# Optimization experiments

Measured on AMD Instinct MI355X. Metric: run time of the kernel, lower is better.

## Reference

```python
import math
import jax, jax.numpy as jnp
import numpy as np

N_HEAD = 8
BLOCK_SIZE = 1024
LN_EPS = 1e-5


def _layer_norm(x, g, b):
    mu = jnp.mean(x, axis=-1, keepdims=True)
    var = jnp.var(x, axis=-1, keepdims=True)
    return (x - mu) * jax.lax.rsqrt(var + LN_EPS) * g + b


def _skew(QEr):
    # QEr: (B, nh, L, L) -> pad one zero column on the left, reshape, drop first row
    B, nh, nr, nc = QEr.shape
    padded = jnp.pad(QEr, ((0, 0), (0, 0), (0, 0), (1, 0)))  # (B, nh, nr, nc+1)
    reshaped = padded.reshape(B, nh, nc + 1, nr)
    return reshaped[:, :, 1:, :]  # (B, nh, nr, nc)


def _attn(x, W_qkv, b_qkv, W_o, b_o, Er):
    B, L, D = x.shape
    hs = D // N_HEAD
    qkv = x @ W_qkv + b_qkv  # (B, L, 3D)
    q, k, v = jnp.split(qkv, 3, axis=-1)
    # (B, nh, L, hs)
    q = q.reshape(B, L, N_HEAD, hs).transpose(0, 2, 1, 3)
    k = k.reshape(B, L, N_HEAD, hs).transpose(0, 2, 1, 3)
    v = v.reshape(B, L, N_HEAD, hs).transpose(0, 2, 1, 3)
    start = BLOCK_SIZE - L
    Er_t = Er[start:, :].T  # (hs, L)
    QEr = q @ Er_t  # (B, nh, L, L)
    Srel = _skew(QEr)
    scores = (jnp.einsum('bhqd,bhkd->bhqk', q, k) + Srel) * (1.0 / math.sqrt(hs))
    causal = jnp.tril(jnp.ones((L, L), dtype=bool))
    scores = jnp.where(causal, scores, jnp.float32(-jnp.inf))
    att = jax.nn.softmax(scores, axis=-1)
    y = jnp.einsum('bhqk,bhkd->bhqd', att, v)
    y = y.transpose(0, 2, 1, 3).reshape(B, L, D)
    return y @ W_o + b_o


def reference(x, W_qkv, b_qkv, W_o, b_o, Er, ln1_g, ln1_b, ln2_g, ln2_b,
              W_fc, b_fc, W_proj, b_proj):
    x = x + _attn(_layer_norm(x, ln1_g, ln1_b), W_qkv, b_qkv, W_o, b_o, Er)
    h = _layer_norm(x, ln2_g, ln2_b) @ W_fc + b_fc
    h = jax.nn.gelu(h, approximate=False)
    h = h @ W_proj + b_proj
    return x + h


def setup_inputs() -> dict:
    key = jax.random.key(0)
    ks = jax.random.split(key, 8)
    B, L, D, F = 8, 1024, 1024, 4096
    hs = D // N_HEAD
    s = lambda fan_in: 1.0 / math.sqrt(fan_in)
    return {
        'x': jax.random.normal(ks[0], (B, L, D), dtype=jnp.float32),
        'W_qkv': jax.random.normal(ks[1], (D, 3 * D), dtype=jnp.float32) * s(D),
        'b_qkv': jnp.zeros((3 * D,), dtype=jnp.float32),
        'W_o': jax.random.normal(ks[2], (D, D), dtype=jnp.float32) * s(D),
        'b_o': jnp.zeros((D,), dtype=jnp.float32),
        'Er': jax.random.normal(ks[3], (BLOCK_SIZE, hs), dtype=jnp.float32),
        'ln1_g': jnp.ones((D,), dtype=jnp.float32),
        'ln1_b': jnp.zeros((D,), dtype=jnp.float32),
        'ln2_g': jnp.ones((D,), dtype=jnp.float32),
        'ln2_b': jnp.zeros((D,), dtype=jnp.float32),
        'W_fc': jax.random.normal(ks[4], (D, F), dtype=jnp.float32) * s(D),
        'b_fc': jnp.zeros((F,), dtype=jnp.float32),
        'W_proj': jax.random.normal(ks[5], (F, D), dtype=jnp.float32) * s(F),
        'b_proj': jnp.zeros((D,), dtype=jnp.float32),
    }
```

## Files before the change

kernel.cpp:

```cpp
#include <hip/hip_runtime.h>
#include <hip/hip_bf16.h>
#include <math.h>

#define BB 8
#define LL 1024
#define DD 1024
#define FF 4096
#define NHH 8
#define HSS 128
#define SCALE 0.08838834764831845f
#define TRI(qi, kt) ((qi) * ((qi) + 1) / 2 + (kt))

typedef __bf16 bf16;
typedef __bf16 bf16x8 __attribute__((ext_vector_type(8)));
typedef float f32x4 __attribute__((ext_vector_type(4)));
typedef _Float16 f16;
typedef _Float16 f16x4 __attribute__((ext_vector_type(4)));

__device__ inline void async_copy16(const void* g, void* l) {
  __builtin_amdgcn_global_load_lds(
      (const __attribute__((address_space(1))) unsigned int*)g,
      (__attribute__((address_space(3))) unsigned int*)l, 16, 0, 0);
}

__global__ __launch_bounds__(256)
void transpose_cast_kernel(const float* __restrict__ W, bf16* __restrict__ Wt,
                           int K, int N) {
  __shared__ float tile[32][33];
  int n0 = blockIdx.x * 32, k0 = blockIdx.y * 32;
  int tx = threadIdx.x, ty = threadIdx.y;
#pragma unroll
  for (int i = 0; i < 32; i += 8)
    tile[ty + i][tx] = W[(size_t)(k0 + ty + i) * N + n0 + tx];
  __syncthreads();
#pragma unroll
  for (int i = 0; i < 32; i += 8)
    Wt[(size_t)(n0 + ty + i) * K + k0 + tx] = (bf16)tile[tx][ty + i];
}

__global__ __launch_bounds__(256)
void pack_er_kernel(const float* __restrict__ Er, bf16* __restrict__ ErP) {
  int g = blockIdx.x, tid = threadIdx.x;
  int l15 = tid & 15, quad = (tid >> 4) & 3, st = tid >> 6;
  const float* src = Er + (size_t)(g * 16 + l15) * HSS + st * 32 + quad * 8;
  bf16* dst = ErP + (size_t)g * 2048 + tid * 8;
#pragma unroll
  for (int j = 0; j < 8; j++) dst[j] = (bf16)src[j];
}

__global__ __launch_bounds__(256)
void ln_kernel(const float* __restrict__ x, const float* __restrict__ g,
               const float* __restrict__ bta, bf16* __restrict__ out) {
  int row = blockIdx.x;
  int tid = threadIdx.x;
  const float4 v = ((const float4*)(x + (size_t)row * DD))[tid];
  float s = v.x + v.y + v.z + v.w;
  float s2 = v.x * v.x + v.y * v.y + v.z * v.z + v.w * v.w;
#pragma unroll
  for (int o = 32; o > 0; o >>= 1) {
    s += __shfl_down(s, o);
    s2 += __shfl_down(s2, o);
  }
  __shared__ float a1[4], a2[4];
  int wave = tid >> 6;
  if ((tid & 63) == 0) { a1[wave] = s; a2[wave] = s2; }
  __syncthreads();
  s = a1[0] + a1[1] + a1[2] + a1[3];
  s2 = a2[0] + a2[1] + a2[2] + a2[3];
  float mu = s * (1.0f / DD);
  float rstd = rsqrtf(s2 * (1.0f / DD) - mu * mu + 1e-5f);
  float4 gv = ((const float4*)g)[tid];
  float4 bv = ((const float4*)bta)[tid];
  bf16* o4 = out + (size_t)row * DD + tid * 4;
  o4[0] = (bf16)((v.x - mu) * rstd * gv.x + bv.x);
  o4[1] = (bf16)((v.y - mu) * rstd * gv.y + bv.y);
  o4[2] = (bf16)((v.z - mu) * rstd * gv.z + bv.z);
  o4[3] = (bf16)((v.w - mu) * rstd * gv.w + bv.w);
}

template <int EPI>
__global__ __launch_bounds__(256)
void gemm_kernel(const bf16* __restrict__ A, const bf16* __restrict__ Bt,
                 const float* __restrict__ bias, const float* __restrict__ res,
                 void* __restrict__ Cout, int M, int N, int K) {
  __shared__ bf16 Als[128 * 64];
  __shared__ bf16 Bls[128 * 64];
  int tid = threadIdx.x;
  int wave = tid >> 6, lane = tid & 63;
  int l15 = lane & 15, quad = lane >> 4;

  int m0 = blockIdx.y * 128, n0 = blockIdx.x * 128;
  int wm = (wave >> 1) * 64, wn = (wave & 1) * 64;
  f32x4 acc[4][4] = {};

  const bf16* asrc[4];
  const bf16* bsrc[4];
  int ldso[4];
#pragma unroll
  for (int i = 0; i < 4; i++) {
    int u = i * 256 + tid;
    int row = u >> 3, c = u & 7;
    int g = c ^ (row & 7);
    asrc[i] = A + (size_t)(m0 + row) * K + g * 8;
    bsrc[i] = Bt + (size_t)(n0 + row) * K + g * 8;
    ldso[i] = u * 8;
  }

  for (int k0 = 0; k0 < K; k0 += 64) {
    __syncthreads();
#pragma unroll
    for (int i = 0; i < 4; i++) {
      async_copy16(asrc[i] + k0, &Als[ldso[i]]);
      async_copy16(bsrc[i] + k0, &Bls[ldso[i]]);
    }
    __syncthreads();

    bf16x8 af[2][4], bfr[2][4];
#pragma unroll
    for (int kk = 0; kk < 2; kk++) {
#pragma unroll
      for (int mt = 0; mt < 4; mt++) {
        int ra = wm + mt * 16 + l15;
        af[kk][mt] = *(const bf16x8*)&Als[ra * 64 + (((kk * 4 + quad) ^ (ra & 7)) << 3)];
        int rb = wn + mt * 16 + l15;
        bfr[kk][mt] = *(const bf16x8*)&Bls[rb * 64 + (((kk * 4 + quad) ^ (rb & 7)) << 3)];
      }
    }
#pragma unroll
    for (int kk = 0; kk < 2; kk++)
#pragma unroll
      for (int mt = 0; mt < 4; mt++)
#pragma unroll
        for (int nt = 0; nt < 4; nt++)
          acc[mt][nt] = __builtin_amdgcn_mfma_f32_16x16x32_bf16(af[kk][mt], bfr[kk][nt],
                                                                acc[mt][nt], 0, 0, 0);
  }

#pragma unroll
  for (int mt = 0; mt < 4; mt++) {
#pragma unroll
    for (int nt = 0; nt < 4; nt++) {
      int col = n0 + wn + nt * 16 + l15;
      float bv = bias[col];
#pragma unroll
      for (int r = 0; r < 4; r++) {
        int row = m0 + wm + mt * 16 + quad * 4 + r;
        float v = acc[mt][nt][r] + bv;
        if (EPI == 1) v = 0.5f * v * (1.0f + erff(v * 0.7071067811865475f));
        if (EPI == 2) {
          v += res[(size_t)row * N + col];
          ((float*)Cout)[(size_t)row * N + col] = v;
        } else {
          ((bf16*)Cout)[(size_t)row * N + col] = (bf16)v;
        }
      }
    }
  }
}

__global__ __launch_bounds__(256)
void pack_kv_kernel(const bf16* __restrict__ qkv, bf16* __restrict__ Kpack,
                    bf16* __restrict__ Vpack) {
  __shared__ bf16 Vst[64][132];
  int kt = blockIdx.x, h = blockIdx.y, b = blockIdx.z;
  int tid = threadIdx.x;
  const size_t rs = 3 * DD;
  const bf16* kb = qkv + (size_t)b * LL * rs + (size_t)(kt * 64) * rs + DD + h * HSS;
  const bf16* vb = kb + DD;
  bf16* kp = Kpack + ((size_t)(b * NHH + h) * 16 + kt) * (64 * 128);
  bf16* vp = Vpack + ((size_t)(b * NHH + h) * 16 + kt) * (128 * 64);
#pragma unroll
  for (int i = 0; i < 4; i++) {
    int u = i * 256 + tid;
    int kk = u >> 4, c = u & 15;
    bf16x8 kv = *(const bf16x8*)(kb + (size_t)kk * rs + c * 8);
    *(bf16x8*)(kp + kk * 128 + ((c ^ kk) & 15) * 8) = kv;
    *(bf16x8*)&Vst[kk][c * 8] = *(const bf16x8*)(vb + (size_t)kk * rs + c * 8);
  }
  __syncthreads();
#pragma unroll
  for (int i = 0; i < 4; i++) {
    int u = i * 256 + tid;
    int d = u >> 3, c = u & 7;
    bf16x8 t;
#pragma unroll
    for (int j = 0; j < 8; j++) t[j] = Vst[c * 8 + j][d];
    *(bf16x8*)(vp + d * 64 + ((c ^ (d & 7))) * 8) = t;
  }
}

__global__ __launch_bounds__(256)
void relband_kernel(const bf16* __restrict__ qkv, const bf16* __restrict__ ErP,
                    f16* __restrict__ band) {
  int tid = threadIdx.x, wave = tid >> 6, lane = tid & 63;
  int l15 = lane & 15, quad = lane >> 4;
  int h = blockIdx.y, b = blockIdx.z;
  const size_t rs = 3 * DD;
  const bf16* qbase = qkv + (size_t)b * LL * rs + h * HSS;
  f16* bbase = band + (size_t)(b * NHH + h) * (136 * 4096);

#pragma unroll 1
  for (int ph = 0; ph < 2; ph++) {
    int qb = ph ? 15 - blockIdx.x : blockIdx.x;
    int qw0 = qb * 64 + wave * 16;

    bf16x8 qf[4];
#pragma unroll
    for (int st = 0; st < 4; st++)
      qf[st] = *(const bf16x8*)(qbase + (size_t)(qw0 + l15) * rs + st * 32 + quad * 8);

#pragma unroll 1
    for (int kt = 0; kt <= qb; kt++) {
      int k0 = kt * 64;
      int kmax_off = qw0 + 15 - k0;
      int m_base = 1008 - qw0 + k0;
      int gb = m_base >> 4;
      int ntR = (kmax_off >> 4) + 1;
      if (ntR > 4) ntR = 4;

      f32x4 rr[5] = {};
#pragma unroll
      for (int n = 0; n < 5; n++) {
        if (n <= ntR) {
          int g = gb + n;
          if (g > 63) g = 63;
          const bf16* ep = ErP + (size_t)g * 2048 + lane * 8;
#pragma unroll
          for (int st = 0; st < 4; st++) {
            bf16x8 ef = *(const bf16x8*)(ep + st * 512);
            rr[n] = __builtin_amdgcn_mfma_f32_16x16x32_bf16(qf[st], ef, rr[n], 0, 0, 0);
          }
        }
      }

      f16x4 sf[4];
#pragma unroll
      for (int rg = 0; rg < 4; rg++) {
        int qloc = quad * 4 + rg;
        int tt = 15 - qloc + l15;
        int src = (lane & 48) | (tt & 15);
        float shv[5];
#pragma unroll
        for (int n = 0; n < 5; n++)
          shv[n] = (n <= ntR) ? __shfl(rr[n][rg], src) : 0.f;
#pragma unroll
        for (int nt = 0; nt < 4; nt++)
          sf[nt][rg] = (f16)((tt & 16) ? shv[nt + 1] : shv[nt]);
      }
      f16* tb = bbase + (size_t)TRI(qb, kt) * 4096;
#pragma unroll
      for (int nt = 0; nt < 4; nt++)
        if (nt * 16 <= kmax_off)
          *(f16x4*)(tb + (wave * 4 + nt) * 256 + l15 * 16 + quad * 4) = sf[nt];
    }
  }
}

__global__ __launch_bounds__(256)
void flash_kernel(const bf16* __restrict__ qkv, const bf16* __restrict__ Kpack,
                  const bf16* __restrict__ Vpack, const f16* __restrict__ band,
                  bf16* __restrict__ y) {
  __shared__ bf16 Kls[2][64 * 128];
  __shared__ bf16 Vls[2][128 * 64];
  __shared__ bf16 Pls[4][16][72];

  int tid = threadIdx.x, wave = tid >> 6, lane = tid & 63;
  int l15 = lane & 15, quad = lane >> 4;
  int h = blockIdx.y, b = blockIdx.z;

  const size_t rs = 3 * DD;
  const bf16* qbase = qkv + (size_t)b * LL * rs + h * HSS;
  const bf16* kp = Kpack + (size_t)(b * NHH + h) * 16 * (64 * 128);
  const bf16* vp = Vpack + (size_t)(b * NHH + h) * 16 * (128 * 64);
  const f16* bnd = band + (size_t)(b * NHH + h) * (136 * 4096);

  int buf = 0;
#pragma unroll 1
  for (int ph = 0; ph < 2; ph++) {
    int qb = ph ? 15 - blockIdx.x : blockIdx.x;
    int qw0 = qb * 64 + wave * 16;
    int nkt = qb + 1;

    bf16x8 qf[4];
#pragma unroll
    for (int st = 0; st < 4; st++)
      qf[st] = *(const bf16x8*)(qbase + (size_t)(qw0 + l15) * rs + st * 32 + quad * 8);

    {
      const bf16* ks = kp;
      const bf16* vs = vp;
#pragma unroll
      for (int i = 0; i < 4; i++) {
        int off = (wave * 4 + i) * 512 + lane * 8;
        async_copy16(ks + off, &Kls[buf][off]);
        async_copy16(vs + off, &Vls[buf][off]);
      }
    }

    f32x4 o[8] = {};
    float mrow[4] = {-INFINITY, -INFINITY, -INFINITY, -INFINITY};
    float lrow[4] = {0.f, 0.f, 0.f, 0.f};

#pragma unroll 1
    for (int kt = 0; kt < nkt; kt++) {
      int k0 = kt * 64;
      int kmax_off = qw0 + 15 - k0;
      __syncthreads();

      const f16* tb = bnd + (size_t)TRI(qb, kt) * 4096;
      f16x4 srl[4] = {};
#pragma unroll
      for (int nt = 0; nt < 4; nt++)
        if (nt * 16 <= kmax_off)
          srl[nt] = *(const f16x4*)(tb + (wave * 4 + nt) * 256 + l15 * 16 + quad * 4);

      if (kt + 1 < nkt) {
        const bf16* ks = kp + (size_t)(kt + 1) * (64 * 128);
        const bf16* vs = vp + (size_t)(kt + 1) * (128 * 64);
#pragma unroll
        for (int i = 0; i < 4; i++) {
          int off = (wave * 4 + i) * 512 + lane * 8;
          async_copy16(ks + off, &Kls[buf ^ 1][off]);
          async_copy16(vs + off, &Vls[buf ^ 1][off]);
        }
      }

      f32x4 sa[4] = {};
#pragma unroll
      for (int nt = 0; nt < 4; nt++) {
        if (nt * 16 <= kmax_off) {
          int kk = nt * 16 + l15;
#pragma unroll
          for (int st = 0; st < 4; st++) {
            bf16x8 kf = *(const bf16x8*)&Kls[buf][kk * 128 + (((st * 4 + quad) ^ l15) & 15) * 8];
            sa[nt] = __builtin_amdgcn_mfma_f32_16x16x32_bf16(qf[st], kf, sa[nt], 0, 0, 0);
          }
        }
      }

      float pmx[4] = {-INFINITY, -INFINITY, -INFINITY, -INFINITY};
#pragma unroll
      for (int nt = 0; nt < 4; nt++) {
        if (nt * 16 <= kmax_off) {
          int kg = k0 + nt * 16 + l15;
#pragma unroll
          for (int rg = 0; rg < 4; rg++) {
            int qg = qw0 + quad * 4 + rg;
            float v = (sa[nt][rg] + (float)srl[nt][rg]) * SCALE;
            v = (kg <= qg) ? v : -INFINITY;
            sa[nt][rg] = v;
            pmx[rg] = fmaxf(pmx[rg], v);
          }
        } else {
#pragma unroll
          for (int rg = 0; rg < 4; rg++) sa[nt][rg] = -INFINITY;
        }
      }

#pragma unroll
      for (int rg = 0; rg < 4; rg++) {
        float v = pmx[rg];
        v = fmaxf(v, __shfl_xor(v, 1));
        v = fmaxf(v, __shfl_xor(v, 2));
        v = fmaxf(v, __shfl_xor(v, 4));
        v = fmaxf(v, __shfl_xor(v, 8));
        float mnew = fmaxf(mrow[rg], v);
        float alpha = __expf(mrow[rg] - mnew);
        mrow[rg] = mnew;
        lrow[rg] *= alpha;
#pragma unroll
        for (int nt = 0; nt < 8; nt++) o[nt][rg] *= alpha;
        pmx[rg] = mnew;
      }
      float ls[4] = {0.f, 0.f, 0.f, 0.f};
#pragma unroll
      for (int nt = 0; nt < 4; nt++)
#pragma unroll
        for (int rg = 0; rg < 4; rg++) {
          float p = __expf(sa[nt][rg] - pmx[rg]);
          ls[rg] += p;
          Pls[wave][quad * 4 + rg][nt * 16 + l15] = (bf16)p;
        }
#pragma unroll
      for (int rg = 0; rg < 4; rg++) {
        float v = ls[rg];
        v += __shfl_xor(v, 1);
        v += __shfl_xor(v, 2);
        v += __shfl_xor(v, 4);
        v += __shfl_xor(v, 8);
        lrow[rg] += v;
      }

      bf16x8 pf[2];
#pragma unroll
      for (int s2 = 0; s2 < 2; s2++)
        pf[s2] = *(const bf16x8*)&Pls[wave][l15][s2 * 32 + quad * 8];
#pragma unroll
      for (int nt = 0; nt < 8; nt++) {
        int d = nt * 16 + l15;
#pragma unroll
        for (int s2 = 0; s2 < 2; s2++) {
          if (s2 * 32 <= kmax_off) {
            bf16x8 vf = *(const bf16x8*)&Vls[buf][d * 64 + (((s2 * 4 + quad) ^ (l15 & 7)) & 7) * 8];
            o[nt] = __builtin_amdgcn_mfma_f32_16x16x32_bf16(pf[s2], vf, o[nt], 0, 0, 0);
          }
        }
      }
      buf ^= 1;
    }

#pragma unroll
    for (int rg = 0; rg < 4; rg++) {
      float inv = 1.0f / lrow[rg];
      int qg = qw0 + quad * 4 + rg;
      bf16* yr = y + ((size_t)b * LL + qg) * DD + h * HSS;
#pragma unroll
      for (int nt = 0; nt < 8; nt++) yr[nt * 16 + l15] = (bf16)(o[nt][rg] * inv);
    }
  }
}

extern "C" void kernel_launch(void* const* d_in, const int* in_sizes, int n_in,
                              void* d_out, int out_size, void* d_ws, size_t ws_size,
                              hipStream_t stream) {
  const float* x = (const float*)d_in[0];
  const float* W_qkv = (const float*)d_in[1];
  const float* b_qkv = (const float*)d_in[2];
  const float* W_o = (const float*)d_in[3];
  const float* b_o = (const float*)d_in[4];
  const float* Er = (const float*)d_in[5];
  const float* ln1_g = (const float*)d_in[6];
  const float* ln1_b = (const float*)d_in[7];
  const float* ln2_g = (const float*)d_in[8];
  const float* ln2_b = (const float*)d_in[9];
  const float* W_fc = (const float*)d_in[10];
  const float* b_fc = (const float*)d_in[11];
  const float* W_proj = (const float*)d_in[12];
  const float* b_proj = (const float*)d_in[13];
  float* out = (float*)d_out;

  char* p = (char*)d_ws;
  auto alloc = [&](size_t bytes) {
    char* r = p;
    p += (bytes + 255) & ~(size_t)255;
    return r;
  };
  bf16* Wt_qkv = (bf16*)alloc((size_t)3072 * 1024 * 2);
  bf16* Wt_o   = (bf16*)alloc((size_t)1024 * 1024 * 2);
  bf16* Wt_fc  = (bf16*)alloc((size_t)4096 * 1024 * 2);
  bf16* Wt_pr  = (bf16*)alloc((size_t)1024 * 4096 * 2);
  bf16* ErP    = (bf16*)alloc((size_t)1024 * 128 * 2);
  bf16* xn     = (bf16*)alloc((size_t)8192 * 1024 * 2);
  bf16* qkvb   = (bf16*)alloc((size_t)8192 * 3072 * 2);
  bf16* yb     = (bf16*)alloc((size_t)8192 * 1024 * 2);
  bf16* Kpack  = (bf16*)alloc((size_t)64 * 16 * 64 * 128 * 2);
  bf16* Vpack  = (bf16*)alloc((size_t)64 * 16 * 128 * 64 * 2);
  f16*  band   = (f16*)alloc((size_t)64 * 136 * 4096 * 2);
  float* x2    = (float*)band;
  bf16* hb     = qkvb;

  transpose_cast_kernel<<<dim3(3072 / 32, 1024 / 32), dim3(32, 8), 0, stream>>>(W_qkv, Wt_qkv, 1024, 3072);
  transpose_cast_kernel<<<dim3(1024 / 32, 1024 / 32), dim3(32, 8), 0, stream>>>(W_o, Wt_o, 1024, 1024);
  transpose_cast_kernel<<<dim3(4096 / 32, 1024 / 32), dim3(32, 8), 0, stream>>>(W_fc, Wt_fc, 1024, 4096);
  transpose_cast_kernel<<<dim3(1024 / 32, 4096 / 32), dim3(32, 8), 0, stream>>>(W_proj, Wt_pr, 4096, 1024);
  pack_er_kernel<<<64, 256, 0, stream>>>(Er, ErP);

  ln_kernel<<<8192, 256, 0, stream>>>(x, ln1_g, ln1_b, xn);
  gemm_kernel<0><<<dim3(24, 64), 256, 0, stream>>>(xn, Wt_qkv, b_qkv, nullptr, qkvb, 8192, 3072, 1024);
  pack_kv_kernel<<<dim3(16, 8, 8), 256, 0, stream>>>(qkvb, Kpack, Vpack);
  relband_kernel<<<dim3(8, 8, 8), 256, 0, stream>>>(qkvb, ErP, band);
  flash_kernel<<<dim3(8, 8, 8), 256, 0, stream>>>(qkvb, Kpack, Vpack, band, yb);
  gemm_kernel<2><<<dim3(8, 64), 256, 0, stream>>>(yb, Wt_o, b_o, x, x2, 8192, 1024, 1024);
  ln_kernel<<<8192, 256, 0, stream>>>(x2, ln2_g, ln2_b, xn);
  gemm_kernel<1><<<dim3(32, 64), 256, 0, stream>>>(xn, Wt_fc, b_fc, nullptr, hb, 8192, 4096, 1024);
  gemm_kernel<2><<<dim3(8, 64), 256, 0, stream>>>(hb, Wt_pr, b_proj, x2, out, 8192, 1024, 4096);
}
```

Measured before the change: 616.5 us.

## Add 256x256-tile 8-wave GEMM with ping-pong LDS staging for QKV and FC

Introduces a new GEMM kernel using 256x256 output tiles, 512 threads and double-buffered LDS. It interleaves async global-to-LDS loads of quarter tiles with MFMA phases, using explicit vmcnt waits, barriers and setprio. The kernel replaces the 128x128 GEMM for the QKV projection and the FC+GELU projection, aiming for more data reuse per tile and better overlap of loads with compute. The cost is a large LDS footprint (128KB) and register pressure, which may limit occupancy. Grid sizes also drop, to 384 and 512 blocks.

```diff
diff --git a/kernel.cpp b/kernel.cpp
--- a/kernel.cpp
+++ b/kernel.cpp
@@ -22,6 +22,10 @@
       (const __attribute__((address_space(1))) unsigned int*)g,
       (__attribute__((address_space(3))) unsigned int*)l, 16, 0, 0);
 }
+
+#define FENCE() asm volatile("" ::: "memory")
+#define BARRIER() do { FENCE(); __builtin_amdgcn_s_barrier(); FENCE(); } while (0)
+#define VMCNT6() asm volatile("s_waitcnt vmcnt(6)" ::: "memory")
 
 __global__ __launch_bounds__(256)
 void transpose_cast_kernel(const float* __restrict__ W, bf16* __restrict__ Wt,
@@ -76,6 +80,122 @@
   o4[1] = (bf16)((v.y - mu) * rstd * gv.y + bv.y);
   o4[2] = (bf16)((v.z - mu) * rstd * gv.z + bv.z);
   o4[3] = (bf16)((v.w - mu) * rstd * gv.w + bv.w);
+}
+
+template <int EPI>
+__global__ __launch_bounds__(512)
+void gemm256_kernel(const bf16* __restrict__ A, const bf16* __restrict__ Bt,
+                    const float* __restrict__ bias, void* __restrict__ Cout,
+                    int M, int N, int K) {
+  __shared__ bf16 Als[2][256 * 64];
+  __shared__ bf16 Bls[2][256 * 64];
+  int tid = threadIdx.x;
+  int wave = tid >> 6, lane = tid & 63;
+  int l15 = lane & 15, quad = lane >> 4;
+  int wmi = wave >> 2, wni = wave & 3;
+  int m0 = blockIdx.y * 256, n0 = blockIdx.x * 256;
+
+  int u0 = tid, u1 = tid + 512;
+  int r0 = u0 >> 3, c0 = ((u0 & 7) ^ (r0 & 7)) << 3;
+  int r1 = u1 >> 3, c1 = ((u1 & 7) ^ (r1 & 7)) << 3;
+  const bf16* aB0 = A + (size_t)(m0 + r0) * K + c0;
+  const bf16* aB1 = A + (size_t)(m0 + r1) * K + c1;
+  const bf16* bB0 = Bt + (size_t)(n0 + r0) * K + c0;
+  const bf16* bB1 = Bt + (size_t)(n0 + r1) * K + c1;
+  int d0 = u0 * 8, d1 = u1 * 8;
+
+  auto stageA = [&](int b, int h, int t) {
+    size_t off = (size_t)h * 128 * K + (size_t)t * 64;
+    async_copy16(aB0 + off, &Als[b][h * 8192 + d0]);
+    async_copy16(aB1 + off, &Als[b][h * 8192 + d1]);
+  };
+  auto stageB = [&](int b, int h, int t) {
+    size_t off = (size_t)h * 128 * K + (size_t)t * 64;
+    async_copy16(bB0 + off, &Bls[b][h * 8192 + d0]);
+    async_copy16(bB1 + off, &Bls[b][h * 8192 + d1]);
+  };
+
+  f32x4 acc[8][4] = {};
+  bf16x8 af[2][4], bfr[2][2];
+
+  auto readA = [&](int b, int qm) {
+#pragma unroll
+    for (int kk = 0; kk < 2; kk++)
+#pragma unroll
+      for (int mt = 0; mt < 4; mt++) {
+        int ra = qm * 128 + wmi * 64 + mt * 16 + l15;
+        af[kk][mt] = *(const bf16x8*)&Als[b][ra * 64 + (((kk * 4 + quad) ^ (ra & 7)) << 3)];
+      }
+  };
+  auto readB = [&](int b, int qn) {
+#pragma unroll
+    for (int kk = 0; kk < 2; kk++)
+#pragma unroll
+      for (int nt = 0; nt < 2; nt++) {
+        int rb = qn * 128 + wni * 32 + nt * 16 + l15;
+        bfr[kk][nt] = *(const bf16x8*)&Bls[b][rb * 64 + (((kk * 4 + quad) ^ (rb & 7)) << 3)];
+      }
+  };
+  auto mfma16 = [&](int qm, int qn) {
+    __builtin_amdgcn_s_setprio(1);
+#pragma unroll
+    for (int kk = 0; kk < 2; kk++)
+#pragma unroll
+      for (int mt = 0; mt < 4; mt++)
+#pragma unroll
+        for (int nt = 0; nt < 2; nt++)
+          acc[qm * 4 + mt][qn * 2 + nt] = __builtin_amdgcn_mfma_f32_16x16x32_bf16(
+              af[kk][mt], bfr[kk][nt], acc[qm * 4 + mt][qn * 2 + nt], 0, 0, 0);
+    __builtin_amdgcn_s_setprio(0);
+  };
+
+  int nk = K >> 6;
+  stageA(0, 0, 0); stageB(0, 0, 0); stageB(0, 1, 0); stageA(0, 1, 0);
+  stageA(1, 0, 1); stageB(1, 1, 1);
+  VMCNT6();
+  BARRIER();
+
+  for (int t = 0; t < nk; t++) {
+    int cur = t & 1;
+    readA(cur, 0); readB(cur, 0);
+    if (t + 1 < nk) stageB(cur ^ 1, 0, t + 1);
+    BARRIER();
+    mfma16(0, 0);
+    BARRIER();
+    readB(cur, 1);
+    if (t + 1 < nk) stageA(cur ^ 1, 1, t + 1);
+    VMCNT6();
+    BARRIER();
+    mfma16(0, 1);
+    BARRIER();
+    readA(cur, 1);
+    if (t + 2 < nk) stageA(cur, 0, t + 2);
+    BARRIER();
+    mfma16(1, 1);
+    BARRIER();
+    readB(cur, 0);
+    if (t + 2 < nk) stageB(cur, 1, t + 2);
+    VMCNT6();
+    BARRIER();
+    mfma16(1, 0);
+    BARRIER();
+  }
+
+#pragma unroll
+  for (int MT = 0; MT < 8; MT++) {
+#pragma unroll
+    for (int NT = 0; NT < 4; NT++) {
+      int col = n0 + (NT >> 1) * 128 + wni * 32 + (NT & 1) * 16 + l15;
+      float bv = bias[col];
+#pragma unroll
+      for (int r = 0; r < 4; r++) {
+        int row = m0 + (MT >> 2) * 128 + wmi * 64 + (MT & 3) * 16 + quad * 4 + r;
+        float v = acc[MT][NT][r] + bv;
+        if (EPI == 1) v = 0.5f * v * (1.0f + erff(v * 0.7071067811865475f));
+        ((bf16*)Cout)[(size_t)row * N + col] = (bf16)v;
+      }
+    }
+  }
 }
 
 template <int EPI>
@@ -466,12 +586,12 @@
   pack_er_kernel<<<64, 256, 0, stream>>>(Er, ErP);
 
   ln_kernel<<<8192, 256, 0, stream>>>(x, ln1_g, ln1_b, xn);
-  gemm_kernel<0><<<dim3(24, 64), 256, 0, stream>>>(xn, Wt_qkv, b_qkv, nullptr, qkvb, 8192, 3072, 1024);
+  gemm256_kernel<0><<<dim3(12, 32), 512, 0, stream>>>(xn, Wt_qkv, b_qkv, qkvb, 8192, 3072, 1024);
   pack_kv_kernel<<<dim3(16, 8, 8), 256, 0, stream>>>(qkvb, Kpack, Vpack);
   relband_kernel<<<dim3(8, 8, 8), 256, 0, stream>>>(qkvb, ErP, band);
   flash_kernel<<<dim3(8, 8, 8), 256, 0, stream>>>(qkvb, Kpack, Vpack, band, yb);
   gemm_kernel<2><<<dim3(8, 64), 256, 0, stream>>>(yb, Wt_o, b_o, x, x2, 8192, 1024, 1024);
   ln_kernel<<<8192, 256, 0, stream>>>(x2, ln2_g, ln2_b, xn);
-  gemm_kernel<1><<<dim3(32, 64), 256, 0, stream>>>(xn, Wt_fc, b_fc, nullptr, hb, 8192, 4096, 1024);
+  gemm256_kernel<1><<<dim3(16, 32), 512, 0, stream>>>(xn, Wt_fc, b_fc, hb, 8192, 4096, 1024);
   gemm_kernel<2><<<dim3(8, 64), 256, 0, stream>>>(hb, Wt_pr, b_proj, x2, out, 8192, 1024, 4096);
 }
```

After: 600.3 us. 2.6% less time.
